# Kernel optimization log

Hardware: AMD Instinct MI355X
Metric: run time of the kernel (lower is better)

## Reference

```python
import jax, jax.numpy as jnp
import numpy as np

B, T, C = 16, 4096, 64  # batch, seq_len, n_embd == head_size


def setup_inputs() -> dict:
    key = jax.random.key(0)
    k1, k2, k3, k4 = jax.random.split(key, 4)
    x = jax.random.normal(k1, (B, T, C), dtype=jnp.float32)
    Wq = jax.random.normal(k2, (C, C), dtype=jnp.float32) * (C ** -0.5)
    Wk = jax.random.normal(k3, (C, C), dtype=jnp.float32) * (C ** -0.5)
    Wv = jax.random.normal(k4, (C, C), dtype=jnp.float32) * (C ** -0.5)
    return {"x": x, "Wq": Wq, "Wk": Wk, "Wv": Wv}


def reference(x, Wq, Wk, Wv):
    # Single-head causal self-attention (dropout rate = 0.0 in source -> identity).
    q = jnp.einsum('btc,cd->btd', x, Wq)  # [B,T,D]
    k = jnp.einsum('btc,cd->btd', x, Wk)  # [B,T,D]
    v = jnp.einsum('btc,cd->btd', x, Wv)  # [B,T,D]
    scale = q.shape[-1] ** -0.5
    wei = jnp.einsum('btd,bsd->bts', q, k) * scale  # [B,T,T] scores
    causal = jnp.tril(jnp.ones((T, T), dtype=bool))  # [T,T]
    wei = jnp.where(causal[None, :, :], wei, jnp.finfo(wei.dtype).min)
    wei = jax.nn.softmax(wei, axis=-1)
    out = jnp.einsum('bts,bsd->btd', wei, v)  # [B,T,D]
    return out
```

## Files before the change

### kernel.cpp

```cpp
#include <hip/hip_runtime.h>
#include <hip/hip_bf16.h>
#include <math.h>

#define BATCH 16
#define SEQ 4096
#define HDIM 64

typedef __attribute__((ext_vector_type(8))) short bf16x8;
typedef __attribute__((ext_vector_type(4))) short bf16x4;
typedef __attribute__((ext_vector_type(4))) float f32x4;
typedef __attribute__((ext_vector_type(8))) unsigned short us8;

#define QSCALE 0.1803368801111601f

static __device__ __forceinline__ float exp2_fast(float x) {
#if __has_builtin(__builtin_amdgcn_exp2f)
    return __builtin_amdgcn_exp2f(x);
#else
    float r; asm("v_exp_f32 %0, %1" : "=v"(r) : "v"(x)); return r;
#endif
}

static __device__ __forceinline__ void load_lds16(const void* g, void* l) {
    __builtin_amdgcn_global_load_lds(
        (const __attribute__((address_space(1))) unsigned int*)g,
        (__attribute__((address_space(3))) unsigned int*)l,
        16, 0, 0);
}

static __device__ __forceinline__ unsigned short bf16bits(float f) {
    __hip_bfloat16 h = __float2bfloat16(f);
    return *(unsigned short*)&h;
}

__global__ __launch_bounds__(256)
void qkv_mfma_kernel(const float* __restrict__ x,
                     const float* __restrict__ Wq,
                     const float* __restrict__ Wk,
                     const float* __restrict__ Wv,
                     __hip_bfloat16* __restrict__ qb,
                     __hip_bfloat16* __restrict__ kb,
                     __hip_bfloat16* __restrict__ vt) {
    __shared__ __attribute__((aligned(16))) __hip_bfloat16 swt[3 * 64 * 64];
    __shared__ __attribute__((aligned(16))) __hip_bfloat16 sout[64][80];
    const int tid = threadIdx.x;
    const int wv = tid >> 6;
    const int lane = tid & 63;
    const int quad = lane >> 4;
    const int ml = lane & 15;
    const size_t row0 = (size_t)blockIdx.x * 64;
    const int batch = (int)(row0 >> 12);
    const int t0 = (int)(row0 & 4095);

    #pragma unroll
    for (int mat = 0; mat < 3; ++mat) {
        const float* W = (mat == 0) ? Wq : (mat == 1) ? Wk : Wv;
        const float sc = (mat == 0) ? QSCALE : 1.0f;
        const int n = tid & 63;
        #pragma unroll
        for (int i = 0; i < 16; ++i) {
            const int f = i * 256 + tid;
            const int k = f >> 6;
            swt[mat * 4096 + n * 64 + (((k >> 3) ^ (n & 7)) << 3) + (k & 7)] =
                __float2bfloat16(W[f] * sc);
        }
    }

    bf16x8 a0, a1;
    {
        const float4* xr = (const float4*)(x + (row0 + wv * 16 + ml) * HDIM);
        float4 lo = xr[quad * 2], hi = xr[quad * 2 + 1];
        float t8[8] = {lo.x, lo.y, lo.z, lo.w, hi.x, hi.y, hi.z, hi.w};
        #pragma unroll
        for (int j = 0; j < 8; ++j) a0[j] = (short)bf16bits(t8[j]);
        lo = xr[8 + quad * 2]; hi = xr[9 + quad * 2];
        float u8[8] = {lo.x, lo.y, lo.z, lo.w, hi.x, hi.y, hi.z, hi.w};
        #pragma unroll
        for (int j = 0; j < 8; ++j) a1[j] = (short)bf16bits(u8[j]);
    }
    __syncthreads();

    #pragma unroll
    for (int mat = 0; mat < 3; ++mat) {
        const __hip_bfloat16* wb = swt + mat * 4096;
        f32x4 acc[4];
        #pragma unroll
        for (int nt = 0; nt < 4; ++nt) {
            const int n = nt * 16 + ml;
            const int nx = n & 7;
            const bf16x8 bl = *(const bf16x8*)(wb + (size_t)n * 64 + (size_t)((quad) ^ nx) * 8);
            const bf16x8 bh = *(const bf16x8*)(wb + (size_t)n * 64 + (size_t)((quad + 4) ^ nx) * 8);
            acc[nt] = __builtin_amdgcn_mfma_f32_16x16x32_bf16(a0, bl, (f32x4){0.f,0.f,0.f,0.f}, 0, 0, 0);
            acc[nt] = __builtin_amdgcn_mfma_f32_16x16x32_bf16(a1, bh, acc[nt], 0, 0, 0);
        }

        if (mat < 2) {
            #pragma unroll
            for (int nt = 0; nt < 4; ++nt)
                #pragma unroll
                for (int r = 0; r < 4; ++r)
                    sout[wv * 16 + quad * 4 + r][nt * 16 + ml] = __float2bfloat16(acc[nt][r]);
        } else {
            #pragma unroll
            for (int nt = 0; nt < 4; ++nt)
                #pragma unroll
                for (int r = 0; r < 4; ++r)
                    sout[nt * 16 + ml][wv * 16 + quad * 4 + r] = __float2bfloat16(acc[nt][r]);
        }
        __syncthreads();
        __hip_bfloat16* dst = (mat == 0) ? qb : (mat == 1) ? kb : vt;
        #pragma unroll
        for (int c2 = 0; c2 < 2; ++c2) {
            const int cc = c2 * 256 + tid;
            const int row = cc >> 3, g = cc & 7;
            us8 u = *(const us8*)&sout[row][g * 8];
            if (mat < 2)
                *(us8*)(dst + (row0 + row) * HDIM + g * 8) = u;
            else
                *(us8*)(dst + ((size_t)batch * HDIM + row) * SEQ + t0 + g * 8) = u;
        }
        __syncthreads();
    }
}

__global__ __launch_bounds__(256, 4)
void flash_mfma_kernel(const __hip_bfloat16* __restrict__ qb,
                       const __hip_bfloat16* __restrict__ kbuf,
                       const __hip_bfloat16* __restrict__ vt,
                       float* __restrict__ out) {
    __shared__ __attribute__((aligned(16))) __hip_bfloat16 sk[64 * 64];
    __shared__ __attribute__((aligned(16))) __hip_bfloat16 sv[64 * 64];
    const int tid = threadIdx.x;
    const int wv = tid >> 6;
    const int lane = tid & 63;
    const int quad = lane >> 4;
    const int ml = lane & 15;

    const int id = blockIdx.x;
    const int b = id & 15;
    const int t = id >> 4;
    const int hi2 = t >> 4, mid = t & 15;
    const int qt = (hi2 == 0) ? (63 - mid)
                 : (hi2 == 1) ? (32 + mid)
                 : (hi2 == 2) ? (31 - mid) : mid;
    const int qbase = qt * 64 + wv * 16;
    const size_t bb = (size_t)b * SEQ * HDIM;

    const __hip_bfloat16* Q = qb + bb;
    const __hip_bfloat16* K = kbuf + bb;
    const __hip_bfloat16* VT = vt + bb;

    const bf16x8 a0 = *(const bf16x8*)(Q + (size_t)(qbase + ml) * HDIM + quad * 8);
    const bf16x8 a1 = *(const bf16x8*)(Q + (size_t)(qbase + ml) * HDIM + 32 + quad * 8);

    bf16x8 ones8;
    #pragma unroll
    for (int j = 0; j < 8; ++j) ones8[j] = (short)0x3F80;

    f32x4 acc[4];
    #pragma unroll
    for (int nt = 0; nt < 4; ++nt) acc[nt] = (f32x4){0.f, 0.f, 0.f, 0.f};
    f32x4 lacc = (f32x4){0.f, 0.f, 0.f, 0.f};

    const int s0 = wv * 128 + lane;
    const int s1 = s0 + 64;
    const int r0row = s0 >> 3, r0ch = (s0 & 7) ^ (r0row & 7);
    const int r1row = s1 >> 3, r1ch = (s1 & 7) ^ (r1row & 7);
    __hip_bfloat16* ldsb0k = sk + (size_t)(wv * 128) * 8;
    __hip_bfloat16* ldsb1k = sk + (size_t)(wv * 128 + 64) * 8;
    __hip_bfloat16* ldsb0v = sv + (size_t)(wv * 128) * 8;
    __hip_bfloat16* ldsb1v = sv + (size_t)(wv * 128 + 64) * 8;

    const int ntiles = qt + 1;
    for (int tile = 0; tile < ntiles; ++tile) {
        const int kb0 = tile * 64;
        __syncthreads();
        load_lds16(K + (size_t)(kb0 + r0row) * HDIM + r0ch * 8, ldsb0k);
        load_lds16(K + (size_t)(kb0 + r1row) * HDIM + r1ch * 8, ldsb1k);
        load_lds16(VT + (size_t)r0row * SEQ + kb0 + r0ch * 8, ldsb0v);
        load_lds16(VT + (size_t)r1row * SEQ + kb0 + r1ch * 8, ldsb1v);
        asm volatile("s_waitcnt vmcnt(0)" ::: "memory");
        __syncthreads();

        f32x4 st[4];
        #pragma unroll
        for (int tt = 0; tt < 4; ++tt) {
            const int row = tt * 16 + ml;
            const int rb = row << 3, rx = row & 7;
            const bf16x8 kl = *(const bf16x8*)(sk + (size_t)((rb | (quad ^ rx)) * 8));
            const bf16x8 kh = *(const bf16x8*)(sk + (size_t)((rb | ((quad + 4) ^ rx)) * 8));
            st[tt] = __builtin_amdgcn_mfma_f32_16x16x32_bf16(kl, a0, (f32x4){0.f,0.f,0.f,0.f}, 0, 0, 0);
            st[tt] = __builtin_amdgcn_mfma_f32_16x16x32_bf16(kh, a1, st[tt], 0, 0, 0);
        }

        const bool edge = (tile == qt);
        const int q = qbase + ml;
        bf16x8 p8[2];
        #pragma unroll
        for (int tt2 = 0; tt2 < 2; ++tt2) {
            #pragma unroll
            for (int half = 0; half < 2; ++half) {
                const int tt = tt2 * 2 + half;
                #pragma unroll
                for (int r = 0; r < 4; ++r) {
                    const int key = kb0 + tt * 16 + quad * 4 + r;
                    float pv = exp2_fast(st[tt][r]);
                    if (edge && (key > q)) pv = 0.f;
                    p8[tt2][half * 4 + r] = (short)bf16bits(pv);
                }
            }
        }

        lacc = __builtin_amdgcn_mfma_f32_16x16x32_bf16(ones8, p8[0], lacc, 0, 0, 0);
        lacc = __builtin_amdgcn_mfma_f32_16x16x32_bf16(ones8, p8[1], lacc, 0, 0, 0);

        #pragma unroll
        for (int tt2 = 0; tt2 < 2; ++tt2) {
            #pragma unroll
            for (int nt = 0; nt < 4; ++nt) {
                const int row = nt * 16 + ml;
                const int rx = row & 7;
                const int c0 = 4 * tt2 + (quad >> 1);
                const char* base = (const char*)sv + (size_t)row * 128 + (quad & 1) * 8;
                const bf16x4 vlo = *(const bf16x4*)(base + ((c0 ^ rx) * 16));
                const bf16x4 vhi = *(const bf16x4*)(base + (((c0 + 2) ^ rx) * 16));
                bf16x8 va;
                #pragma unroll
                for (int j = 0; j < 4; ++j) { va[j] = vlo[j]; va[4 + j] = vhi[j]; }
                acc[nt] = __builtin_amdgcn_mfma_f32_16x16x32_bf16(va, p8[tt2], acc[nt], 0, 0, 0);
            }
        }
    }

    const float inv = 1.0f / lacc[0];
    float* orow = out + bb + (size_t)(qbase + ml) * HDIM;
    #pragma unroll
    for (int nt = 0; nt < 4; ++nt) {
        float4 o;
        o.x = acc[nt][0] * inv; o.y = acc[nt][1] * inv;
        o.z = acc[nt][2] * inv; o.w = acc[nt][3] * inv;
        *(float4*)(orow + nt * 16 + quad * 4) = o;
    }
}

extern "C" void kernel_launch(void* const* d_in, const int* in_sizes, int n_in,
                              void* d_out, int out_size, void* d_ws, size_t ws_size,
                              hipStream_t stream) {
    const float* x  = (const float*)d_in[0];
    const float* Wq = (const float*)d_in[1];
    const float* Wk = (const float*)d_in[2];
    const float* Wv = (const float*)d_in[3];
    float* outp = (float*)d_out;

    const size_t elems = (size_t)BATCH * SEQ * HDIM;
    __hip_bfloat16* qb = (__hip_bfloat16*)d_ws;
    __hip_bfloat16* kb = qb + elems;
    __hip_bfloat16* vt = kb + elems;

    qkv_mfma_kernel<<<dim3(BATCH * SEQ / 64), 256, 0, stream>>>(x, Wq, Wk, Wv, qb, kb, vt);
    flash_mfma_kernel<<<dim3(BATCH * SEQ / 64), 256, 0, stream>>>(qb, kb, vt, outp);
}
```

Before: 144.1 us.

## Split key tile across warp pairs with 32-row queries and LDS merge

Each warp now handles 32 query rows and half of each 64-key tile instead of 16 query rows and the full tile, and the two key-halves are combined through an LDS merge buffer at the end. The V-transpose store permutes columns so each lane gets a contiguous bf16x8 V fragment, replacing the two 4-element loads plus shuffle. One warp per block skips the fully masked diagonal key half. This is meant to improve K/V fragment reuse across query rows and cut LDS traffic, at the cost of more accumulator registers and an extra merge phase with syncs.

```diff
diff --git a/kernel.cpp b/kernel.cpp
--- a/kernel.cpp
+++ b/kernel.cpp
@@ -7,7 +7,6 @@
 #define HDIM 64
 
 typedef __attribute__((ext_vector_type(8))) short bf16x8;
-typedef __attribute__((ext_vector_type(4))) short bf16x4;
 typedef __attribute__((ext_vector_type(4))) float f32x4;
 typedef __attribute__((ext_vector_type(8))) unsigned short us8;
 
@@ -105,7 +104,8 @@
             for (int nt = 0; nt < 4; ++nt)
                 #pragma unroll
                 for (int r = 0; r < 4; ++r)
-                    sout[nt * 16 + ml][wv * 16 + quad * 4 + r] = __float2bfloat16(acc[nt][r]);
+                    sout[nt * 16 + ml][(wv >> 1) * 32 + quad * 8 + (wv & 1) * 4 + r] =
+                        __float2bfloat16(acc[nt][r]);
         }
         __syncthreads();
         __hip_bfloat16* dst = (mat == 0) ? qb : (mat == 1) ? kb : vt;
@@ -130,11 +130,14 @@
                        float* __restrict__ out) {
     __shared__ __attribute__((aligned(16))) __hip_bfloat16 sk[64 * 64];
     __shared__ __attribute__((aligned(16))) __hip_bfloat16 sv[64 * 64];
+    __shared__ __attribute__((aligned(16))) float smerge[2][64][18];
     const int tid = threadIdx.x;
     const int wv = tid >> 6;
     const int lane = tid & 63;
     const int quad = lane >> 4;
     const int ml = lane & 15;
+    const int mh = wv & 1;
+    const int kh = wv >> 1;
 
     const int id = blockIdx.x;
     const int b = id & 15;
@@ -143,24 +146,30 @@
     const int qt = (hi2 == 0) ? (63 - mid)
                  : (hi2 == 1) ? (32 + mid)
                  : (hi2 == 2) ? (31 - mid) : mid;
-    const int qbase = qt * 64 + wv * 16;
+    const int qbw = qt * 64 + mh * 32;
     const size_t bb = (size_t)b * SEQ * HDIM;
 
     const __hip_bfloat16* Q = qb + bb;
     const __hip_bfloat16* K = kbuf + bb;
     const __hip_bfloat16* VT = vt + bb;
 
-    const bf16x8 a0 = *(const bf16x8*)(Q + (size_t)(qbase + ml) * HDIM + quad * 8);
-    const bf16x8 a1 = *(const bf16x8*)(Q + (size_t)(qbase + ml) * HDIM + 32 + quad * 8);
+    bf16x8 bq[2][2];
+    #pragma unroll
+    for (int qi = 0; qi < 2; ++qi)
+        #pragma unroll
+        for (int h = 0; h < 2; ++h)
+            bq[qi][h] = *(const bf16x8*)(Q + (size_t)(qbw + qi * 16 + ml) * HDIM + h * 32 + quad * 8);
 
     bf16x8 ones8;
     #pragma unroll
     for (int j = 0; j < 8; ++j) ones8[j] = (short)0x3F80;
 
-    f32x4 acc[4];
-    #pragma unroll
-    for (int nt = 0; nt < 4; ++nt) acc[nt] = (f32x4){0.f, 0.f, 0.f, 0.f};
-    f32x4 lacc = (f32x4){0.f, 0.f, 0.f, 0.f};
+    f32x4 acc[4][2];
+    #pragma unroll
+    for (int nt = 0; nt < 4; ++nt)
+        #pragma unroll
+        for (int qi = 0; qi < 2; ++qi) acc[nt][qi] = (f32x4){0.f, 0.f, 0.f, 0.f};
+    f32x4 lacc[2] = {(f32x4){0.f,0.f,0.f,0.f}, (f32x4){0.f,0.f,0.f,0.f}};
 
     const int s0 = wv * 128 + lane;
     const int s1 = s0 + 64;
@@ -171,6 +180,7 @@
     __hip_bfloat16* ldsb0v = sv + (size_t)(wv * 128) * 8;
     __hip_bfloat16* ldsb1v = sv + (size_t)(wv * 128 + 64) * 8;
 
+    const int rx = ml & 7;
     const int ntiles = qt + 1;
     for (int tile = 0; tile < ntiles; ++tile) {
         const int kb0 = tile * 64;
@@ -182,64 +192,76 @@
         asm volatile("s_waitcnt vmcnt(0)" ::: "memory");
         __syncthreads();
 
-        f32x4 st[4];
-        #pragma unroll
-        for (int tt = 0; tt < 4; ++tt) {
-            const int row = tt * 16 + ml;
-            const int rb = row << 3, rx = row & 7;
-            const bf16x8 kl = *(const bf16x8*)(sk + (size_t)((rb | (quad ^ rx)) * 8));
-            const bf16x8 kh = *(const bf16x8*)(sk + (size_t)((rb | ((quad + 4) ^ rx)) * 8));
-            st[tt] = __builtin_amdgcn_mfma_f32_16x16x32_bf16(kl, a0, (f32x4){0.f,0.f,0.f,0.f}, 0, 0, 0);
-            st[tt] = __builtin_amdgcn_mfma_f32_16x16x32_bf16(kh, a1, st[tt], 0, 0, 0);
+        if (tile == qt && kh == 1 && mh == 0) continue;
+
+        f32x4 st[2][2];
+        #pragma unroll
+        for (int kt = 0; kt < 2; ++kt) {
+            const int row = kh * 32 + kt * 16 + ml;
+            const int rb = row << 3, rxx = row & 7;
+            const bf16x8 kl = *(const bf16x8*)(sk + (size_t)((rb | (quad ^ rxx)) * 8));
+            const bf16x8 khi = *(const bf16x8*)(sk + (size_t)((rb | ((quad + 4) ^ rxx)) * 8));
+            #pragma unroll
+            for (int qi = 0; qi < 2; ++qi) {
+                st[kt][qi] = __builtin_amdgcn_mfma_f32_16x16x32_bf16(kl, bq[qi][0], (f32x4){0.f,0.f,0.f,0.f}, 0, 0, 0);
+                st[kt][qi] = __builtin_amdgcn_mfma_f32_16x16x32_bf16(khi, bq[qi][1], st[kt][qi], 0, 0, 0);
+            }
         }
 
         const bool edge = (tile == qt);
-        const int q = qbase + ml;
         bf16x8 p8[2];
         #pragma unroll
-        for (int tt2 = 0; tt2 < 2; ++tt2) {
-            #pragma unroll
-            for (int half = 0; half < 2; ++half) {
-                const int tt = tt2 * 2 + half;
+        for (int qi = 0; qi < 2; ++qi) {
+            const int q = qbw + qi * 16 + ml;
+            #pragma unroll
+            for (int half = 0; half < 2; ++half)
                 #pragma unroll
                 for (int r = 0; r < 4; ++r) {
-                    const int key = kb0 + tt * 16 + quad * 4 + r;
-                    float pv = exp2_fast(st[tt][r]);
+                    const int key = kb0 + kh * 32 + half * 16 + quad * 4 + r;
+                    float pv = exp2_fast(st[half][qi][r]);
                     if (edge && (key > q)) pv = 0.f;
-                    p8[tt2][half * 4 + r] = (short)bf16bits(pv);
+                    p8[qi][half * 4 + r] = (short)bf16bits(pv);
                 }
+        }
+
+        lacc[0] = __builtin_amdgcn_mfma_f32_16x16x32_bf16(ones8, p8[0], lacc[0], 0, 0, 0);
+        lacc[1] = __builtin_amdgcn_mfma_f32_16x16x32_bf16(ones8, p8[1], lacc[1], 0, 0, 0);
+        #pragma unroll
+        for (int nt = 0; nt < 4; ++nt) {
+            const int row = nt * 16 + ml;
+            const int rb = row << 3, rxx = row & 7;
+            const bf16x8 va = *(const bf16x8*)(sv + (size_t)((rb | ((kh * 4 + quad) ^ rxx)) * 8));
+            acc[nt][0] = __builtin_amdgcn_mfma_f32_16x16x32_bf16(va, p8[0], acc[nt][0], 0, 0, 0);
+            acc[nt][1] = __builtin_amdgcn_mfma_f32_16x16x32_bf16(va, p8[1], acc[nt][1], 0, 0, 0);
+        }
+    }
+
+    #pragma unroll
+    for (int qi = 0; qi < 2; ++qi) {
+        __syncthreads();
+        if (kh == 1) {
+            float* mrow = smerge[mh][lane];
+            #pragma unroll
+            for (int nt = 0; nt < 4; ++nt)
+                #pragma unroll
+                for (int r = 0; r < 4; ++r) mrow[nt * 4 + r] = acc[nt][qi][r];
+            mrow[16] = lacc[qi][0];
+        }
+        __syncthreads();
+        if (kh == 0) {
+            const float* mrow = smerge[mh][lane];
+            const float inv = 1.0f / (lacc[qi][0] + mrow[16]);
+            float* orow = out + bb + (size_t)(qbw + qi * 16 + ml) * HDIM;
+            #pragma unroll
+            for (int nt = 0; nt < 4; ++nt) {
+                float4 o;
+                o.x = (acc[nt][qi][0] + mrow[nt * 4 + 0]) * inv;
+                o.y = (acc[nt][qi][1] + mrow[nt * 4 + 1]) * inv;
+                o.z = (acc[nt][qi][2] + mrow[nt * 4 + 2]) * inv;
+                o.w = (acc[nt][qi][3] + mrow[nt * 4 + 3]) * inv;
+                *(float4*)(orow + nt * 16 + quad * 4) = o;
             }
         }
-
-        lacc = __builtin_amdgcn_mfma_f32_16x16x32_bf16(ones8, p8[0], lacc, 0, 0, 0);
-        lacc = __builtin_amdgcn_mfma_f32_16x16x32_bf16(ones8, p8[1], lacc, 0, 0, 0);
-
-        #pragma unroll
-        for (int tt2 = 0; tt2 < 2; ++tt2) {
-            #pragma unroll
-            for (int nt = 0; nt < 4; ++nt) {
-                const int row = nt * 16 + ml;
-                const int rx = row & 7;
-                const int c0 = 4 * tt2 + (quad >> 1);
-                const char* base = (const char*)sv + (size_t)row * 128 + (quad & 1) * 8;
-                const bf16x4 vlo = *(const bf16x4*)(base + ((c0 ^ rx) * 16));
-                const bf16x4 vhi = *(const bf16x4*)(base + (((c0 + 2) ^ rx) * 16));
-                bf16x8 va;
-                #pragma unroll
-                for (int j = 0; j < 4; ++j) { va[j] = vlo[j]; va[4 + j] = vhi[j]; }
-                acc[nt] = __builtin_amdgcn_mfma_f32_16x16x32_bf16(va, p8[tt2], acc[nt], 0, 0, 0);
-            }
-        }
-    }
-
-    const float inv = 1.0f / lacc[0];
-    float* orow = out + bb + (size_t)(qbase + ml) * HDIM;
-    #pragma unroll
-    for (int nt = 0; nt < 4; ++nt) {
-        float4 o;
-        o.x = acc[nt][0] * inv; o.y = acc[nt][1] * inv;
-        o.z = acc[nt][2] * inv; o.w = acc[nt][3] * inv;
-        *(float4*)(orow + nt * 16 + quad * 4) = o;
     }
 }
 
```

Result: faster. 129.7 us (-10.0%).
